# Kernel optimization log

Hardware: AMD Instinct MI355X
Metric: run time of the kernel (lower is better)

The kernel has to match this reference:

```python
import jax, jax.numpy as jnp
import numpy as np

EMB = 1024
HEADS = 16
HEAD_DIM = EMB // HEADS
D_FF = 4 * EMB
EPS = 1e-5


def setup_inputs() -> dict:
    key = jax.random.key(0)
    ks = jax.random.split(key, 12)
    b, t = 4, 2048
    sc = 0.02
    return {
        "x": jax.random.normal(ks[0], (b, t, EMB), dtype=jnp.float32),
        # weights stored [in, out] (transpose of torch Linear.weight)
        "w_attn": jax.random.normal(ks[1], (EMB, 3 * EMB), dtype=jnp.float32) * sc,
        "b_attn": jnp.zeros((3 * EMB,), dtype=jnp.float32),
        "w_proj": jax.random.normal(ks[2], (EMB, EMB), dtype=jnp.float32) * sc,
        "b_proj": jnp.zeros((EMB,), dtype=jnp.float32),
        "ln1_g": jnp.ones((EMB,), dtype=jnp.float32),
        "ln1_b": jnp.zeros((EMB,), dtype=jnp.float32),
        "w_ff1": jax.random.normal(ks[3], (EMB, D_FF), dtype=jnp.float32) * sc,
        "b_ff1": jnp.zeros((D_FF,), dtype=jnp.float32),
        "w_ff2": jax.random.normal(ks[4], (D_FF, EMB), dtype=jnp.float32) * sc,
        "b_ff2": jnp.zeros((EMB,), dtype=jnp.float32),
        "ln2_g": jnp.ones((EMB,), dtype=jnp.float32),
        "ln2_b": jnp.zeros((EMB,), dtype=jnp.float32),
    }


def _layernorm(x, g, b):
    mu = jnp.mean(x, axis=-1, keepdims=True)
    var = jnp.var(x, axis=-1, keepdims=True)
    return (x - mu) * jax.lax.rsqrt(var + EPS) * g + b


def reference(x, w_attn, b_attn, w_proj, b_proj, ln1_g, ln1_b,
              w_ff1, b_ff1, w_ff2, b_ff2, ln2_g, ln2_b):
    b, t, e = x.shape
    h, s = HEADS, HEAD_DIM
    # fused qkv projection (GPT2-style c_attn)
    qkv = x @ w_attn + b_attn                      # [b, t, 3e]
    q, k, v = jnp.split(qkv, 3, axis=-1)
    q = q.reshape(b, t, h, s).transpose(0, 2, 1, 3)  # [b, h, t, s]
    k = k.reshape(b, t, h, s).transpose(0, 2, 1, 3)
    v = v.reshape(b, t, h, s).transpose(0, 2, 1, 3)
    dot = jnp.einsum('bhqs,bhks->bhqk', q, k) / jnp.sqrt(jnp.float32(s))
    # causal mask: mask_(..., mask_diagonal=False) zeroes i < j (strict upper)
    causal = jnp.tril(jnp.ones((t, t), dtype=bool))
    dot = jnp.where(causal, dot, jnp.float32(-jnp.inf))
    att = jax.nn.softmax(dot, axis=-1)
    out = jnp.einsum('bhqk,bhks->bhqs', att, v)    # [b, h, t, s]
    out = out.transpose(0, 2, 1, 3).reshape(b, t, e)
    attended = out @ w_proj + b_proj
    # residual + LayerNorm (dropout is identity in eval mode)
    x1 = _layernorm(attended + x, ln1_g, ln1_b)
    ff = jax.nn.relu(x1 @ w_ff1 + b_ff1) @ w_ff2 + b_ff2
    return _layernorm(ff + x1, ln2_g, ln2_b)
```

## Files before the change

kernel.cpp:

```cpp
#include <hip/hip_runtime.h>
#include <hip/hip_bf16.h>


typedef __attribute__((ext_vector_type(8))) short bf16x8;
typedef __attribute__((ext_vector_type(4))) float f32x4;

__device__ __forceinline__ unsigned short f2b(float f) {
  unsigned int u = __float_as_uint(f);
  u += 0x7fffu + ((u >> 16) & 1u);
  return (unsigned short)(u >> 16);
}
__device__ __forceinline__ unsigned int pk2b(float a, float b) {
  __hip_bfloat162 h = __float22bfloat162_rn(make_float2(a, b));
  return *(unsigned int*)&h;
}
__device__ __forceinline__ void gload_lds16(const unsigned short* g, unsigned short* l) {
  __builtin_amdgcn_global_load_lds((const __attribute__((address_space(1))) void*)g,
                                   (__attribute__((address_space(3))) void*)l, 16, 0, 0);
}

__global__ __launch_bounds__(256) void cvt_bf16(const float* __restrict__ in,
                                                unsigned short* __restrict__ out, long n) {
  long i = ((long)blockIdx.x * 256 + threadIdx.x) * 4;
  if (i >= n) return;
  float4 v = *(const float4*)(in + i);
  *(ushort4*)(out + i) = make_ushort4(f2b(v.x), f2b(v.y), f2b(v.z), f2b(v.w));
}

__global__ __launch_bounds__(256) void transpose_bf16(const float* __restrict__ in,
                                                      unsigned short* __restrict__ out,
                                                      int R, int C) {
  __shared__ float tile[32][33];
  int c0 = blockIdx.x * 32, r0 = blockIdx.y * 32;
  for (int i = threadIdx.y; i < 32; i += 8)
    tile[i][threadIdx.x] = in[(long)(r0 + i) * C + c0 + threadIdx.x];
  __syncthreads();
  for (int i = threadIdx.y; i < 32; i += 8)
    out[(long)(c0 + i) * R + r0 + threadIdx.x] = f2b(tile[threadIdx.x][i]);
}

template <int EPI>
__global__ __launch_bounds__(512, 2) void gemm256(const unsigned short* __restrict__ A,
                                                  const unsigned short* __restrict__ Bt,
                                                  const float* __restrict__ bias,
                                                  void* __restrict__ Cout,
                                                  void* __restrict__ Cout2,
                                                  int N, int K, int Kstride) {
  __shared__ __align__(16) unsigned short As[4][256 * 32];
  __shared__ __align__(16) unsigned short Bs[4][256 * 32];

  int tid = threadIdx.x;
  int wv = tid >> 6, lane = tid & 63, quad = lane >> 4, l16 = lane & 15;
  int wm = wv >> 2, wn = wv & 3;

  int nwg = gridDim.x, id = blockIdx.x;
  int sid = (id & 7) * (nwg >> 3) + (id >> 3);
  int bm256 = (sid & 31) * 256, bn256 = (sid >> 5) * 256;
  int chunk = blockIdx.y;
  long kbase = (long)chunk * K;

  int row1 = tid >> 2, row2 = row1 + 128;
  long dsl = ((tid & 3) ^ ((tid >> 3) & 3)) * 8;
  const unsigned short* Ap1 = A + (long)(bm256 + row1) * Kstride + kbase + dsl;
  const unsigned short* Ap2 = A + (long)(bm256 + row2) * Kstride + kbase + dsl;
  const unsigned short* Bp1 = Bt + (long)(bn256 + row1) * Kstride + kbase + dsl;
  const unsigned short* Bp2 = Bt + (long)(bn256 + row2) * Kstride + kbase + dsl;
  int lo1 = wv * 512, lo2 = wv * 512 + 4096;

  f32x4 acc[8][4] = {};
  int sl8 = (quad ^ ((l16 >> 1) & 3)) * 8;
  int arow = wm * 128 + l16;
  int brow = wn * 64 + l16;

  int NT = K >> 5;
  gload_lds16(Ap1, &As[0][lo1]); gload_lds16(Ap2, &As[0][lo2]);
  gload_lds16(Bp1, &Bs[0][lo1]); gload_lds16(Bp2, &Bs[0][lo2]);
  gload_lds16(Ap1 + 32, &As[1][lo1]); gload_lds16(Ap2 + 32, &As[1][lo2]);
  gload_lds16(Bp1 + 32, &Bs[1][lo1]); gload_lds16(Bp2 + 32, &Bs[1][lo2]);
  gload_lds16(Ap1 + 64, &As[2][lo1]); gload_lds16(Ap2 + 64, &As[2][lo2]);
  asm volatile("s_waitcnt vmcnt(6)\n\ts_barrier" ::: "memory");
  __builtin_amdgcn_sched_barrier(0);

  for (int tau = 0; tau < NT; ++tau) {
    const unsigned short* Ab = &As[tau & 3][0];
    const unsigned short* Bb = &Bs[tau & 3][0];
    bf16x8 af[4], bfr[4];
#pragma unroll
    for (int i = 0; i < 4; ++i)
      af[i] = *(const bf16x8*)(Ab + (arow + i * 16) * 32 + sl8);
#pragma unroll
    for (int j = 0; j < 4; ++j)
      bfr[j] = *(const bf16x8*)(Bb + (brow + j * 16) * 32 + sl8);
    if (tau + 2 < NT) {
      long ko = (long)(tau + 2) * 32;
      int s = (tau + 2) & 3;
      gload_lds16(Bp1 + ko, &Bs[s][lo1]);
      gload_lds16(Bp2 + ko, &Bs[s][lo2]);
    }
    asm volatile("s_barrier\n\ts_waitcnt lgkmcnt(0)" ::: "memory");
    __builtin_amdgcn_sched_barrier(0);
    __builtin_amdgcn_s_setprio(1);
#pragma unroll
    for (int i = 0; i < 4; ++i)
#pragma unroll
      for (int j = 0; j < 4; ++j)
        acc[i][j] = __builtin_amdgcn_mfma_f32_16x16x32_bf16(af[i], bfr[j], acc[i][j], 0, 0, 0);
    __builtin_amdgcn_s_setprio(0);
    __builtin_amdgcn_s_barrier();
    __builtin_amdgcn_sched_barrier(0);
    bf16x8 ag[4];
#pragma unroll
    for (int i = 0; i < 4; ++i)
      ag[i] = *(const bf16x8*)(Ab + (arow + (i + 4) * 16) * 32 + sl8);
    if (tau + 3 < NT) {
      long ko = (long)(tau + 3) * 32;
      int s = (tau + 3) & 3;
      gload_lds16(Ap1 + ko, &As[s][lo1]);
      gload_lds16(Ap2 + ko, &As[s][lo2]);
    }
    asm volatile("s_barrier\n\ts_waitcnt lgkmcnt(0)" ::: "memory");
    __builtin_amdgcn_sched_barrier(0);
    __builtin_amdgcn_s_setprio(1);
#pragma unroll
    for (int i = 0; i < 4; ++i)
#pragma unroll
      for (int j = 0; j < 4; ++j)
        acc[i + 4][j] = __builtin_amdgcn_mfma_f32_16x16x32_bf16(ag[i], bfr[j], acc[i + 4][j], 0, 0, 0);
    __builtin_amdgcn_s_setprio(0);
    if (tau + 3 < NT) {
      asm volatile("s_waitcnt vmcnt(6)\n\ts_barrier" ::: "memory");
    } else if (tau + 2 < NT) {
      asm volatile("s_waitcnt vmcnt(4)\n\ts_barrier" ::: "memory");
    } else if (tau + 1 < NT) {
      asm volatile("s_waitcnt vmcnt(0)\n\ts_barrier" ::: "memory");
    }
    __builtin_amdgcn_sched_barrier(0);
  }

  void* Cbase = chunk ? Cout2 : Cout;
#pragma unroll
  for (int i = 0; i < 8; ++i) {
#pragma unroll
    for (int j = 0; j < 4; ++j) {
      int gn = bn256 + wn * 64 + j * 16 + l16;
      float bv = chunk ? 0.f : bias[gn];
      if (EPI == 3 && gn >= 2048) {
        int h = (gn >> 6) & 15, s = gn & 63;
        int gm0 = bm256 + wm * 128 + i * 16 + quad * 4;
        int b = gm0 >> 11, tt0 = gm0 & 2047;
        unsigned short* vt = (unsigned short*)Cout + 16777216L;
        ushort4 us;
        us.x = f2b(acc[i][j][0] + bv);
        us.y = f2b(acc[i][j][1] + bv);
        us.z = f2b(acc[i][j][2] + bv);
        us.w = f2b(acc[i][j][3] + bv);
        *(ushort4*)(vt + (((long)(b * 16 + h)) * 64 + s) * 2048 + tt0) = us;
      } else {
#pragma unroll
        for (int r = 0; r < 4; ++r) {
          int gm = bm256 + wm * 128 + i * 16 + quad * 4 + r;
          float v = acc[i][j][r] + bv;
          if (EPI == 2) v = fmaxf(v, 0.f);
          if (EPI == 0) {
            ((float*)Cbase)[(long)gm * N + gn] = v;
          } else if (EPI == 2) {
            ((unsigned short*)Cbase)[(long)gm * N + gn] = f2b(v);
          } else {
            float sc = (gn < 1024) ? 0.18033688011112042f : 1.0f;
            ((unsigned short*)Cbase)[(long)gm * 2048 + gn] = f2b(v * sc);
          }
        }
      }
    }
  }
}

__global__ __launch_bounds__(256) void attn_mfma(const unsigned short* __restrict__ qkv,
                                                 unsigned short* __restrict__ outp) {
  const int LD = 72;
  __shared__ __align__(16) unsigned short Ks[64 * LD];
  __shared__ __align__(16) unsigned short Vts[64 * LD];
  __shared__ __align__(16) unsigned short Ps[4][32 * LD];
  int id = blockIdx.x;
  int qa = (id >> 3) & 7, qb = 15 - qa;
  int g = (id & 7) | ((id >> 6) << 3);
  int h = g & 15, b = g >> 4;
  int t = threadIdx.x;
  int w = t >> 6, lane = t & 63, quad = lane >> 4, l16 = lane & 15;
  const unsigned short* qg = qkv + (long)(b * 2048) * 2048 + h * 64;
  const unsigned short* kg = qg + 1024;
  const unsigned short* vg = qkv + 16777216L + (((long)(b * 16 + h)) * 64) * 2048;
  unsigned short* Pw = &Ps[w][0];

  bf16x8 qfa[2][2], qfb[2][2];
#pragma unroll
  for (int qq = 0; qq < 2; ++qq)
#pragma unroll
    for (int ks = 0; ks < 2; ++ks) {
      qfa[qq][ks] = *(const bf16x8*)(qg + (long)(qa * 128 + w * 32 + qq * 16 + l16) * 2048 + ks * 32 + quad * 8);
      qfb[qq][ks] = *(const bf16x8*)(qg + (long)(qb * 128 + w * 32 + qq * 16 + l16) * 2048 + ks * 32 + quad * 8);
    }

  int sr = t >> 2, sc = (t & 3) * 16;
  const unsigned short* kp = kg + (long)sr * 2048 + sc;
  const unsigned short* vp = vg + (long)sr * 2048 + sc;
  int4 kv0 = *(const int4*)kp, kv1 = *(const int4*)(kp + 8);
  int4 vv0 = *(const int4*)vp, vv1 = *(const int4*)(vp + 8);
  kp += (long)64 * 2048;
  vp += 64;

  f32x4 oa[2][4] = {}, ob[2][4] = {};
  f32x4 la[2] = {}, lb[2] = {};
  const short ONE = 0x3F80;
  bf16x8 ones = {ONE, ONE, ONE, ONE, ONE, ONE, ONE, ONE};

  auto process = [&](const bf16x8 (&qf)[2][2], int qt2, int kt,
                     f32x4 (&oacc)[2][4], f32x4 (&lacc)[2]) {
    int rel = kt - qt2;
    bool diag = (rel >= 0);
    int off = rel << 6;
#pragma unroll
    for (int rg = 0; rg < 4; ++rg) {
      bf16x8 kf0 = *(const bf16x8*)(Ks + (rg * 16 + l16) * LD + quad * 8);
      bf16x8 kf1 = *(const bf16x8*)(Ks + (rg * 16 + l16) * LD + 32 + quad * 8);
#pragma unroll
      for (int qq = 0; qq < 2; ++qq) {
        f32x4 st = {};
        st = __builtin_amdgcn_mfma_f32_16x16x32_bf16(kf0, qf[qq][0], st, 0, 0, 0);
        st = __builtin_amdgcn_mfma_f32_16x16x32_bf16(kf1, qf[qq][1], st, 0, 0, 0);
        if (diag) {
          int kq = rg * 16 + quad * 4 + off;
          int qrow = w * 32 + qq * 16 + l16;
#pragma unroll
          for (int r = 0; r < 4; ++r)
            if (kq + r > qrow) st[r] = -1e30f;
        }
        unsigned int lo = pk2b(exp2f(st[0]), exp2f(st[1]));
        unsigned int hi = pk2b(exp2f(st[2]), exp2f(st[3]));
        *(uint2*)(Pw + (qq * 16 + l16) * LD + rg * 16 + quad * 4) = make_uint2(lo, hi);
      }
    }
#pragma unroll
    for (int kc = 0; kc < 2; ++kc) {
      bf16x8 ap0 = *(const bf16x8*)(Pw + l16 * LD + kc * 32 + quad * 8);
      bf16x8 ap1 = *(const bf16x8*)(Pw + (16 + l16) * LD + kc * 32 + quad * 8);
      lacc[0] = __builtin_amdgcn_mfma_f32_16x16x32_bf16(ap0, ones, lacc[0], 0, 0, 0);
      lacc[1] = __builtin_amdgcn_mfma_f32_16x16x32_bf16(ap1, ones, lacc[1], 0, 0, 0);
#pragma unroll
      for (int sg = 0; sg < 4; ++sg) {
        bf16x8 vf = *(const bf16x8*)(Vts + (sg * 16 + l16) * LD + kc * 32 + quad * 8);
        oacc[0][sg] = __builtin_amdgcn_mfma_f32_16x16x32_bf16(ap0, vf, oacc[0][sg], 0, 0, 0);
        oacc[1][sg] = __builtin_amdgcn_mfma_f32_16x16x32_bf16(ap1, vf, oacc[1][sg], 0, 0, 0);
      }
    }
  };

  int nkt = 2 * qb + 2;
  for (int kt = 0; kt < nkt; ++kt) {
    __syncthreads();
    *(int4*)(Ks + sr * LD + sc) = kv0;
    *(int4*)(Ks + sr * LD + sc + 8) = kv1;
    *(int4*)(Vts + sr * LD + sc) = vv0;
    *(int4*)(Vts + sr * LD + sc + 8) = vv1;
    __syncthreads();
    if (kt + 1 < nkt) {
      kv0 = *(const int4*)kp; kv1 = *(const int4*)(kp + 8);
      vv0 = *(const int4*)vp; vv1 = *(const int4*)(vp + 8);
      kp += (long)64 * 2048;
      vp += 64;
    }
    process(qfb, 2 * qb, kt, ob, lb);
    if (kt <= 2 * qa + 1) process(qfa, 2 * qa, kt, oa, la);
  }

  auto epi = [&](int qt, f32x4 (&oacc)[2][4], f32x4 (&lacc)[2]) {
#pragma unroll
    for (int qq = 0; qq < 2; ++qq)
#pragma unroll
      for (int r = 0; r < 4; ++r) {
        float invl = 1.f / lacc[qq][r];
        int row = qt * 128 + w * 32 + qq * 16 + quad * 4 + r;
        unsigned short* op = outp + ((long)(b * 2048 + row)) * 1024 + h * 64;
#pragma unroll
        for (int sg = 0; sg < 4; ++sg) op[sg * 16 + l16] = f2b(oacc[qq][sg][r] * invl);
      }
  };
  epi(qa, oa, la);
  epi(qb, ob, lb);
}

__global__ __launch_bounds__(256) void ln_kernel(const float* __restrict__ a,
                                                 const float* __restrict__ a2,
                                                 const float* __restrict__ res,
                                                 const float* __restrict__ gam,
                                                 const float* __restrict__ bet,
                                                 float* __restrict__ outf,
                                                 unsigned short* __restrict__ outb) {
  int row = blockIdx.x, t = threadIdx.x;
  float4 av = *(const float4*)(a + (long)row * 1024 + t * 4);
  float4 rv = *(const float4*)(res + (long)row * 1024 + t * 4);
  float v0 = av.x + rv.x, v1 = av.y + rv.y, v2 = av.z + rv.z, v3 = av.w + rv.w;
  if (a2) {
    float4 a2v = *(const float4*)(a2 + (long)row * 1024 + t * 4);
    v0 += a2v.x; v1 += a2v.y; v2 += a2v.z; v3 += a2v.w;
  }
  float s = v0 + v1 + v2 + v3;
  float ss = v0 * v0 + v1 * v1 + v2 * v2 + v3 * v3;
#pragma unroll
  for (int off = 32; off >= 1; off >>= 1) {
    s += __shfl_down(s, off);
    ss += __shfl_down(ss, off);
  }
  __shared__ float sb[4], ssb[4];
  __shared__ float mean_s, inv_s;
  int w = t >> 6, lane = t & 63;
  if (lane == 0) { sb[w] = s; ssb[w] = ss; }
  __syncthreads();
  if (t == 0) {
    float S = sb[0] + sb[1] + sb[2] + sb[3];
    float SS = ssb[0] + ssb[1] + ssb[2] + ssb[3];
    float mean = S * (1.f / 1024.f);
    float var = SS * (1.f / 1024.f) - mean * mean;
    mean_s = mean;
    inv_s = rsqrtf(var + 1e-5f);
  }
  __syncthreads();
  float mean = mean_s, inv = inv_s;
  int c = t * 4;
  float4 gv = *(const float4*)(gam + c);
  float4 bv = *(const float4*)(bet + c);
  float y0 = (v0 - mean) * inv * gv.x + bv.x;
  float y1 = (v1 - mean) * inv * gv.y + bv.y;
  float y2 = (v2 - mean) * inv * gv.z + bv.z;
  float y3 = (v3 - mean) * inv * gv.w + bv.w;
  *(float4*)(outf + (long)row * 1024 + c) = make_float4(y0, y1, y2, y3);
  if (outb) {
    *(ushort4*)(outb + (long)row * 1024 + c) = make_ushort4(f2b(y0), f2b(y1), f2b(y2), f2b(y3));
  }
}

extern "C" void kernel_launch(void* const* d_in, const int* in_sizes, int n_in,
                              void* d_out, int out_size, void* d_ws, size_t ws_size,
                              hipStream_t stream) {
  const float* x      = (const float*)d_in[0];
  const float* w_attn = (const float*)d_in[1];
  const float* b_attn = (const float*)d_in[2];
  const float* w_proj = (const float*)d_in[3];
  const float* b_proj = (const float*)d_in[4];
  const float* ln1_g  = (const float*)d_in[5];
  const float* ln1_b  = (const float*)d_in[6];
  const float* w_ff1  = (const float*)d_in[7];
  const float* b_ff1  = (const float*)d_in[8];
  const float* w_ff2  = (const float*)d_in[9];
  const float* b_ff2  = (const float*)d_in[10];
  const float* ln2_g  = (const float*)d_in[11];
  const float* ln2_b  = (const float*)d_in[12];

  const long M = 8192, E = 1024;
  char* ws = (char*)d_ws;
  unsigned short* xb   = (unsigned short*)ws; ws += M * E * 2;
  unsigned short* wTa  = (unsigned short*)ws; ws += 3072L * 1024 * 2;
  unsigned short* wTp  = (unsigned short*)ws; ws += 1024L * 1024 * 2;
  unsigned short* wTf1 = (unsigned short*)ws; ws += 4096L * 1024 * 2;
  unsigned short* wTf2 = (unsigned short*)ws; ws += 4096L * 1024 * 2;
  unsigned short* qkvb = (unsigned short*)ws; ws += M * 3072 * 2;
  unsigned short* attb = (unsigned short*)ws; ws += M * E * 2;
  float* a1f = (float*)ws; ws += M * E * 4;
  float* x1f = (float*)ws; ws += M * E * 4;
  unsigned short* x1b = (unsigned short*)ws; ws += M * E * 2;
  unsigned short* hb = qkvb;
  float* f2 = a1f;
  float* prj1 = (float*)qkvb;
  float* ff21 = (float*)d_ws;

  cvt_bf16<<<dim3((M * E) / 4 / 256), dim3(256), 0, stream>>>(x, xb, M * E);
  transpose_bf16<<<dim3(3072 / 32, 1024 / 32), dim3(32, 8), 0, stream>>>(w_attn, wTa, 1024, 3072);
  transpose_bf16<<<dim3(1024 / 32, 1024 / 32), dim3(32, 8), 0, stream>>>(w_proj, wTp, 1024, 1024);
  transpose_bf16<<<dim3(4096 / 32, 1024 / 32), dim3(32, 8), 0, stream>>>(w_ff1, wTf1, 1024, 4096);
  transpose_bf16<<<dim3(1024 / 32, 4096 / 32), dim3(32, 8), 0, stream>>>(w_ff2, wTf2, 4096, 1024);
  gemm256<3><<<dim3(384, 1), dim3(512), 0, stream>>>(xb, wTa, b_attn, qkvb, nullptr, 3072, 1024, 1024);
  attn_mfma<<<dim3(512), dim3(256), 0, stream>>>(qkvb, attb);
  gemm256<0><<<dim3(128, 2), dim3(512), 0, stream>>>(attb, wTp, b_proj, a1f, prj1, 1024, 512, 1024);
  ln_kernel<<<dim3(8192), dim3(256), 0, stream>>>(a1f, prj1, x, ln1_g, ln1_b, x1f, x1b);
  gemm256<2><<<dim3(512, 1), dim3(512), 0, stream>>>(x1b, wTf1, b_ff1, hb, nullptr, 4096, 1024, 1024);
  gemm256<0><<<dim3(128, 2), dim3(512), 0, stream>>>(hb, wTf2, b_ff2, f2, ff21, 1024, 2048, 4096);
  ln_kernel<<<dim3(8192), dim3(256), 0, stream>>>(f2, ff21, x1f, ln2_g, ln2_b, (float*)d_out, nullptr);
}
```

Before: 585.6 us.

## Keep attention P in registers, swizzle and double-buffer K/V LDS tiles

The attention kernel drops the per-warp LDS round trip for the softmax probability tile. It permutes which K rows each MFMA computes so the S-accumulator output already matches the A-operand layout needed for the PV MFMA, and packs it directly in registers. K and V tiles move to unpadded 64-wide rows with an XOR swizzle to avoid bank conflicts, and are double-buffered so one barrier per iteration suffices. This frees LDS and removes LDS writes and reads plus a sync, but relies on the row permutation being consistent with the causal mask indices.

After: 571.7 us. -2.4%, faster.

```diff
diff --git a/kernel.cpp b/kernel.cpp
--- a/kernel.cpp
+++ b/kernel.cpp
@@ -177,10 +177,8 @@
 
 __global__ __launch_bounds__(256) void attn_mfma(const unsigned short* __restrict__ qkv,
                                                  unsigned short* __restrict__ outp) {
-  const int LD = 72;
-  __shared__ __align__(16) unsigned short Ks[64 * LD];
-  __shared__ __align__(16) unsigned short Vts[64 * LD];
-  __shared__ __align__(16) unsigned short Ps[4][32 * LD];
+  __shared__ __align__(16) unsigned short Ks[2][64 * 64];
+  __shared__ __align__(16) unsigned short Vts[2][64 * 64];
   int id = blockIdx.x;
   int qa = (id >> 3) & 7, qb = 15 - qa;
   int g = (id & 7) | ((id >> 6) << 3);
@@ -190,7 +188,6 @@
   const unsigned short* qg = qkv + (long)(b * 2048) * 2048 + h * 64;
   const unsigned short* kg = qg + 1024;
   const unsigned short* vg = qkv + 16777216L + (((long)(b * 16 + h)) * 64) * 2048;
-  unsigned short* Pw = &Ps[w][0];
 
   bf16x8 qfa[2][2], qfb[2][2];
 #pragma unroll
@@ -201,9 +198,12 @@
       qfb[qq][ks] = *(const bf16x8*)(qg + (long)(qb * 128 + w * 32 + qq * 16 + l16) * 2048 + ks * 32 + quad * 8);
     }
 
-  int sr = t >> 2, sc = (t & 3) * 16;
-  const unsigned short* kp = kg + (long)sr * 2048 + sc;
-  const unsigned short* vp = vg + (long)sr * 2048 + sc;
+  int sr = t >> 2, c4 = t & 3;
+  int fsr = (sr & 3) | (((sr >> 3) & 1) << 2);
+  int ws0 = sr * 64 + (((2 * c4) ^ fsr) * 8);
+  int ws1 = sr * 64 + (((2 * c4 + 1) ^ fsr) * 8);
+  const unsigned short* kp = kg + (long)sr * 2048 + c4 * 16;
+  const unsigned short* vp = vg + (long)sr * 2048 + c4 * 16;
   int4 kv0 = *(const int4*)kp, kv1 = *(const int4*)(kp + 8);
   int4 vv0 = *(const int4*)vp, vv1 = *(const int4*)(vp + 8);
   kp += (long)64 * 2048;
@@ -214,54 +214,63 @@
   const short ONE = 0x3F80;
   bf16x8 ones = {ONE, ONE, ONE, ONE, ONE, ONE, ONE, ONE};
 
+  int fs = l16 & 7;
+  int fv = (l16 & 3) | (((l16 >> 3) & 1) << 2);
+
   auto process = [&](const bf16x8 (&qf)[2][2], int qt2, int kt,
-                     f32x4 (&oacc)[2][4], f32x4 (&lacc)[2]) {
+                     f32x4 (&oacc)[2][4], f32x4 (&lacc)[2],
+                     const unsigned short* Kb, const unsigned short* Vb) {
     int rel = kt - qt2;
     bool diag = (rel >= 0);
     int off = rel << 6;
 #pragma unroll
-    for (int rg = 0; rg < 4; ++rg) {
-      bf16x8 kf0 = *(const bf16x8*)(Ks + (rg * 16 + l16) * LD + quad * 8);
-      bf16x8 kf1 = *(const bf16x8*)(Ks + (rg * 16 + l16) * LD + 32 + quad * 8);
-#pragma unroll
-      for (int qq = 0; qq < 2; ++qq) {
-        f32x4 st = {};
-        st = __builtin_amdgcn_mfma_f32_16x16x32_bf16(kf0, qf[qq][0], st, 0, 0, 0);
-        st = __builtin_amdgcn_mfma_f32_16x16x32_bf16(kf1, qf[qq][1], st, 0, 0, 0);
-        if (diag) {
-          int kq = rg * 16 + quad * 4 + off;
-          int qrow = w * 32 + qq * 16 + l16;
-#pragma unroll
-          for (int r = 0; r < 4; ++r)
-            if (kq + r > qrow) st[r] = -1e30f;
+    for (int kc = 0; kc < 2; ++kc) {
+      unsigned int apw[2][4];
+#pragma unroll
+      for (int aa = 0; aa < 2; ++aa) {
+        int row = 8 * (l16 >> 2) + (l16 & 3) + 4 * aa + 32 * kc;
+        const unsigned short* kr = Kb + row * 64;
+        bf16x8 kf0 = *(const bf16x8*)(kr + (quad ^ fs) * 8);
+        bf16x8 kf1 = *(const bf16x8*)(kr + ((quad ^ 4 ^ fs)) * 8);
+#pragma unroll
+        for (int qq = 0; qq < 2; ++qq) {
+          f32x4 st = {};
+          st = __builtin_amdgcn_mfma_f32_16x16x32_bf16(kf0, qf[qq][0], st, 0, 0, 0);
+          st = __builtin_amdgcn_mfma_f32_16x16x32_bf16(kf1, qf[qq][1], st, 0, 0, 0);
+          if (diag) {
+            int kq = 8 * quad + 4 * aa + 32 * kc + off;
+            int qrow = w * 32 + qq * 16 + l16;
+#pragma unroll
+            for (int r = 0; r < 4; ++r)
+              if (kq + r > qrow) st[r] = -1e30f;
+          }
+          apw[qq][aa * 2]     = pk2b(exp2f(st[0]), exp2f(st[1]));
+          apw[qq][aa * 2 + 1] = pk2b(exp2f(st[2]), exp2f(st[3]));
         }
-        unsigned int lo = pk2b(exp2f(st[0]), exp2f(st[1]));
-        unsigned int hi = pk2b(exp2f(st[2]), exp2f(st[3]));
-        *(uint2*)(Pw + (qq * 16 + l16) * LD + rg * 16 + quad * 4) = make_uint2(lo, hi);
       }
-    }
-#pragma unroll
-    for (int kc = 0; kc < 2; ++kc) {
-      bf16x8 ap0 = *(const bf16x8*)(Pw + l16 * LD + kc * 32 + quad * 8);
-      bf16x8 ap1 = *(const bf16x8*)(Pw + (16 + l16) * LD + kc * 32 + quad * 8);
-      lacc[0] = __builtin_amdgcn_mfma_f32_16x16x32_bf16(ap0, ones, lacc[0], 0, 0, 0);
-      lacc[1] = __builtin_amdgcn_mfma_f32_16x16x32_bf16(ap1, ones, lacc[1], 0, 0, 0);
+      union { unsigned int u[4]; bf16x8 v; } ap0, ap1;
+#pragma unroll
+      for (int u = 0; u < 4; ++u) { ap0.u[u] = apw[0][u]; ap1.u[u] = apw[1][u]; }
+      lacc[0] = __builtin_amdgcn_mfma_f32_16x16x32_bf16(ap0.v, ones, lacc[0], 0, 0, 0);
+      lacc[1] = __builtin_amdgcn_mfma_f32_16x16x32_bf16(ap1.v, ones, lacc[1], 0, 0, 0);
 #pragma unroll
       for (int sg = 0; sg < 4; ++sg) {
-        bf16x8 vf = *(const bf16x8*)(Vts + (sg * 16 + l16) * LD + kc * 32 + quad * 8);
-        oacc[0][sg] = __builtin_amdgcn_mfma_f32_16x16x32_bf16(ap0, vf, oacc[0][sg], 0, 0, 0);
-        oacc[1][sg] = __builtin_amdgcn_mfma_f32_16x16x32_bf16(ap1, vf, oacc[1][sg], 0, 0, 0);
+        int vrow = sg * 16 + l16;
+        bf16x8 vf = *(const bf16x8*)(Vb + vrow * 64 + (((4 * kc + quad) ^ fv) * 8));
+        oacc[0][sg] = __builtin_amdgcn_mfma_f32_16x16x32_bf16(ap0.v, vf, oacc[0][sg], 0, 0, 0);
+        oacc[1][sg] = __builtin_amdgcn_mfma_f32_16x16x32_bf16(ap1.v, vf, oacc[1][sg], 0, 0, 0);
       }
     }
   };
 
   int nkt = 2 * qb + 2;
   for (int kt = 0; kt < nkt; ++kt) {
-    __syncthreads();
-    *(int4*)(Ks + sr * LD + sc) = kv0;
-    *(int4*)(Ks + sr * LD + sc + 8) = kv1;
-    *(int4*)(Vts + sr * LD + sc) = vv0;
-    *(int4*)(Vts + sr * LD + sc + 8) = vv1;
+    unsigned short* Kb = &Ks[kt & 1][0];
+    unsigned short* Vb = &Vts[kt & 1][0];
+    *(int4*)(Kb + ws0) = kv0;
+    *(int4*)(Kb + ws1) = kv1;
+    *(int4*)(Vb + ws0) = vv0;
+    *(int4*)(Vb + ws1) = vv1;
     __syncthreads();
     if (kt + 1 < nkt) {
       kv0 = *(const int4*)kp; kv1 = *(const int4*)(kp + 8);
@@ -269,8 +278,8 @@
       kp += (long)64 * 2048;
       vp += 64;
     }
-    process(qfb, 2 * qb, kt, ob, lb);
-    if (kt <= 2 * qa + 1) process(qfa, 2 * qa, kt, oa, la);
+    process(qfb, 2 * qb, kt, ob, lb, Kb, Vb);
+    if (kt <= 2 * qa + 1) process(qfa, 2 * qa, kt, oa, la, Kb, Vb);
   }
 
   auto epi = [&](int qt, f32x4 (&oacc)[2][4], f32x4 (&lacc)[2]) {
```
